# Kernel optimization log

Hardware: AMD Instinct MI355X
Metric: run time of the kernel (lower is better)

The kernel has to match this reference:

```python
import jax, jax.numpy as jnp
import numpy as np

B, C, H, N = 4, 128, 4, 2048
D = C // H  # head_dim = 32
BN_EPS = 1e-5


def _conv1(w, b, x):
    # 1x1 Conv1d: [O,C] x [B,C,N] -> [B,O,N]
    return jnp.einsum('oc,bcn->bon', w, x) + b[None, :, None]


def setup_inputs() -> dict:
    key = jax.random.key(0)
    ks = jax.random.split(key, 20)
    p = lambda k, shape: jax.random.normal(k, shape, dtype=jnp.float32) * 0.05
    return {
        'x1': jax.random.normal(ks[0], (B, C, N), dtype=jnp.float32),
        'x2': jax.random.normal(ks[1], (B, C, N), dtype=jnp.float32),
        'kv_mask': jnp.ones((B, N), dtype=bool),
        'wq': p(ks[2], (C, C)), 'bq': p(ks[3], (C,)),
        'wk': p(ks[4], (C, C)), 'bk': p(ks[5], (C,)),
        'wv': p(ks[6], (C, C)), 'bv': p(ks[7], (C,)),
        'wm': p(ks[8], (C, C)), 'bm': p(ks[9], (C,)),
        'wc1': p(ks[10], (2 * C, 2 * C)), 'bc1': p(ks[11], (2 * C,)),
        'bn_gamma': jnp.ones((2 * C,), dtype=jnp.float32),
        'bn_beta': jnp.zeros((2 * C,), dtype=jnp.float32),
        'bn_mean': p(ks[12], (2 * C,)),
        'bn_var': jax.random.uniform(ks[13], (2 * C,), dtype=jnp.float32, minval=0.5, maxval=1.5),
        'wc2': p(ks[14], (C, 2 * C)), 'bc2': p(ks[15], (C,)),
    }


def reference(x1, x2, kv_mask, wq, bq, wk, bk, wv, bv, wm, bm,
              wc1, bc1, bn_gamma, bn_beta, bn_mean, bn_var, wc2, bc2):
    b, _, n = x1.shape
    q = _conv1(wq, bq, x1).reshape(b, H, D, n)   # bhdn
    k = _conv1(wk, bk, x2).reshape(b, H, D, -1)  # bhdm
    v = _conv1(wv, bv, x2).reshape(b, H, D, -1)  # bhdm
    qk = jnp.einsum('bhdn,bhdm->bhnm', q, k)
    # masked_fill on raw QK before scaling, matching torch code
    qk = jnp.where(kv_mask[:, None, None, :], qk, jnp.float32(-1e6))
    score = jax.nn.softmax(qk * (1.0 / D ** 0.5), axis=-1)
    add_value = jnp.einsum('bhnm,bhdm->bhdn', score, v).reshape(b, C, n)
    add_value = _conv1(wm, bm, add_value)
    cat = jnp.concatenate([x1, add_value], axis=1)  # [B, 2C, N]
    h = _conv1(wc1, bc1, cat)
    # BatchNorm1d in inference mode (running stats)
    h = (h - bn_mean[None, :, None]) * jax.lax.rsqrt(bn_var[None, :, None] + BN_EPS)
    h = h * bn_gamma[None, :, None] + bn_beta[None, :, None]
    h = jax.nn.relu(h)
    h = _conv1(wc2, bc2, h)
    return x1 + h
```

## Files before the change

### kernel.cpp

```cpp
#include <hip/hip_runtime.h>

typedef __attribute__((ext_vector_type(4))) float v4f;
typedef __attribute__((ext_vector_type(8))) _Float16 half8;
typedef __attribute__((ext_vector_type(4))) _Float16 half4;
typedef __attribute__((ext_vector_type(2))) _Float16 half2t;

constexpr float C2 = 0.17677669529663687f * 1.44269504088896341f;

__device__ __forceinline__ half4 pk4(float a, float b, float c, float d) {
  half2t lo = __builtin_bit_cast(half2t, __builtin_amdgcn_cvt_pkrtz(a, b));
  half2t hi = __builtin_bit_cast(half2t, __builtin_amdgcn_cvt_pkrtz(c, d));
  return __builtin_shufflevector(lo, hi, 0, 1, 2, 3);
}
__device__ __forceinline__ half8 pk8f4(const float4 a, const float4 b) {
  const half4 lo = pk4(a.x, a.y, a.z, a.w);
  const half4 hi = pk4(b.x, b.y, b.z, b.w);
  return __builtin_shufflevector(lo, hi, 0, 1, 2, 3, 4, 5, 6, 7);
}

__global__ __launch_bounds__(512) void qkv(
    const float* __restrict__ x1, const float* __restrict__ x2,
    const float* __restrict__ wq, const float* __restrict__ bq,
    const float* __restrict__ wk, const float* __restrict__ bk,
    const float* __restrict__ wv, const float* __restrict__ bv,
    const float* __restrict__ wm, const float* __restrict__ wc1,
    const float* __restrict__ wc2, const unsigned char* __restrict__ mask,
    _Float16* __restrict__ Qpk, _Float16* __restrict__ Kpk,
    _Float16* __restrict__ Vpk, _Float16* __restrict__ wts,
    float* __restrict__ maskf) {
  const int b = blockIdx.y;
  const int bx = blockIdx.x;
  const int tid = threadIdx.x, w = tid >> 6, lane = tid & 63;
  const int l = lane & 15, q = lane >> 4;
  const int n0 = bx * 16;
  const int n = n0 + l;

  __shared__ _Float16 x1s[16 * 136];
  __shared__ _Float16 x2s[16 * 136];

  if (b == 0 && bx < 72) {
    const int e = (bx * 512 + tid) * 4;
    const float* src;
    int base;
    if (e < 16384) { src = wm; base = 0; }
    else if (e < 81920) { src = wc1; base = 16384; }
    else { src = wc2; base = 81920; }
    const float4 t = *(const float4*)(src + (e - base));
    *(half4*)(wts + e) = pk4(t.x, t.y, t.z, t.w);
  } else if (b == 1 && bx < 4) {
    const int e = (bx * 512 + tid) * 4;
    const unsigned mv = *(const unsigned*)(mask + e);
    float4 o;
    o.x = (mv & 0x000000ffu) ? 0.f : -1.0e6f * C2;
    o.y = (mv & 0x0000ff00u) ? 0.f : -1.0e6f * C2;
    o.z = (mv & 0x00ff0000u) ? 0.f : -1.0e6f * C2;
    o.w = (mv & 0xff000000u) ? 0.f : -1.0e6f * C2;
    *(float4*)(maskf + e) = o;
  }

  {
    const int ch = tid >> 2, seg = tid & 3;
    const float4 a = *(const float4*)(x1 + (size_t)(b * 128 + ch) * 2048 + n0 + seg * 4);
    const float4 c = *(const float4*)(x2 + (size_t)(b * 128 + ch) * 2048 + n0 + seg * 4);
    x1s[(seg * 4 + 0) * 136 + ch] = (_Float16)a.x;
    x1s[(seg * 4 + 1) * 136 + ch] = (_Float16)a.y;
    x1s[(seg * 4 + 2) * 136 + ch] = (_Float16)a.z;
    x1s[(seg * 4 + 3) * 136 + ch] = (_Float16)a.w;
    x2s[(seg * 4 + 0) * 136 + ch] = (_Float16)c.x;
    x2s[(seg * 4 + 1) * 136 + ch] = (_Float16)c.y;
    x2s[(seg * 4 + 2) * 136 + ch] = (_Float16)c.z;
    x2s[(seg * 4 + 3) * 136 + ch] = (_Float16)c.w;
  }
  __syncthreads();

  half8 x1f[4], x2f[4];
#pragma unroll
  for (int kt = 0; kt < 4; ++kt) {
    x1f[kt] = *(const half8*)&x1s[l * 136 + kt * 32 + q * 8];
    x2f[kt] = *(const half8*)&x2s[l * 136 + kt * 32 + q * 8];
  }

#pragma unroll
  for (int i = 0; i < 3; ++i) {
    const int t = w * 3 + i;
    if (t < 8) {
      const int mt = t;
      v4f acc = *(const v4f*)(bq + mt * 16 + q * 4);
#pragma unroll
      for (int kt = 0; kt < 4; ++kt) {
        const float4 wa = *(const float4*)(wq + (mt * 16 + l) * 128 + kt * 32 + q * 8);
        const float4 wb = *(const float4*)(wq + (mt * 16 + l) * 128 + kt * 32 + q * 8 + 4);
        acc = __builtin_amdgcn_mfma_f32_16x16x32_f16(pk8f4(wa, wb), x1f[kt], acc, 0, 0, 0);
      }
      *(half4*)(Qpk + ((size_t)(b * 8 + mt) * 2048 + n) * 16 + q * 4) =
          pk4(acc[0] * C2, acc[1] * C2, acc[2] * C2, acc[3] * C2);
    } else if (t < 16) {
      const int mt = t - 8;
      v4f acc = *(const v4f*)(bk + mt * 16 + q * 4);
#pragma unroll
      for (int kt = 0; kt < 4; ++kt) {
        const float4 wa = *(const float4*)(wk + (mt * 16 + l) * 128 + kt * 32 + q * 8);
        const float4 wb = *(const float4*)(wk + (mt * 16 + l) * 128 + kt * 32 + q * 8 + 4);
        acc = __builtin_amdgcn_mfma_f32_16x16x32_f16(pk8f4(wa, wb), x2f[kt], acc, 0, 0, 0);
      }
      *(half4*)(Kpk + ((size_t)(b * 8 + mt) * 2048 + n) * 16 + q * 4) =
          pk4(acc[0], acc[1], acc[2], acc[3]);
    } else {
      const int ot = t - 16;
      const float bvv = bv[ot * 16 + l];
      v4f acc = {bvv, bvv, bvv, bvv};
#pragma unroll
      for (int kt = 0; kt < 4; ++kt) {
        const float4 wa = *(const float4*)(wv + (ot * 16 + l) * 128 + kt * 32 + q * 8);
        const float4 wb = *(const float4*)(wv + (ot * 16 + l) * 128 + kt * 32 + q * 8 + 4);
        acc = __builtin_amdgcn_mfma_f32_16x16x32_f16(x2f[kt], pk8f4(wa, wb), acc, 0, 0, 0);
      }
      *(half4*)(Vpk + (((size_t)(b * 4 + (ot >> 1)) * 128 + bx) * 32 +
                       (ot & 1) * 16 + l) * 16 + q * 4) =
          pk4(acc[0], acc[1], acc[2], acc[3]);
    }
  }
}

__global__ __launch_bounds__(256) void attn(
    const _Float16* __restrict__ Qpk, const _Float16* __restrict__ Kpk,
    const _Float16* __restrict__ Vpk, const float* __restrict__ maskf,
    _Float16* __restrict__ Opk, float* __restrict__ lsump) {
  const int bh = blockIdx.y, b = bh >> 2, h = bh & 3;
  const int part = blockIdx.z;
  const int tid = threadIdx.x, w = tid >> 6, lane = tid & 63;
  const int l = lane & 15, q = lane >> 4;
  const int nb = blockIdx.x * 128 + w * 32;

  __shared__ _Float16 ldsK[2][3088];
  __shared__ _Float16 ldsV[2][3072];

  const size_t qrow = (size_t)(b * 8 + h * 2 + (q >> 1)) * 2048;
  const half8 qf0 = *(const half8*)(Qpk + (qrow + nb + l) * 16 + (q & 1) * 8);
  const half8 qf1 = *(const half8*)(Qpk + (qrow + nb + 16 + l) * 16 + (q & 1) * 8);
  const _Float16* __restrict__ Kg = Kpk + (size_t)(b * 8 + h * 2) * 2048 * 16;
  const _Float16* __restrict__ Vg = Vpk + (size_t)((b * 4 + h) * 128) * 512;
  const float* __restrict__ mf = maskf + b * 2048;

  const int kct = tid >> 7, kk = (tid >> 1) & 63, khf = tid & 1;
  const int vt = tid >> 6, vd = (tid >> 1) & 31;

  v4f oacc[2][2] = {{{0.f, 0.f, 0.f, 0.f}, {0.f, 0.f, 0.f, 0.f}},
                    {{0.f, 0.f, 0.f, 0.f}, {0.f, 0.f, 0.f, 0.f}}};
  float ls0 = 0.f, ls1 = 0.f;
  const int mbeg = part * 512;

  half8 kr = *(const half8*)(Kg + ((size_t)kct * 2048 + mbeg + kk) * 16 + khf * 8);
  half8 vr = *(const half8*)(Vg + (size_t)((mbeg >> 4) + vt) * 512 + vd * 16 + khf * 8);
  *(half8*)&ldsK[0][kct * 1544 + kk * 24 + khf * 8] = kr;
  *(half8*)&ldsV[0][vt * 768 + vd * 24 + khf * 8] = vr;
  __syncthreads();

  for (int i = 0; i < 8; ++i) {
    const int m0 = mbeg + i * 64;
    const int cur = i & 1;
    if (i < 7) {
      kr = *(const half8*)(Kg + ((size_t)kct * 2048 + m0 + 64 + kk) * 16 + khf * 8);
      vr = *(const half8*)(Vg + (size_t)(((m0 + 64) >> 4) + vt) * 512 + vd * 16 + khf * 8);
    }
    half4 pB[2][4];
#pragma unroll
    for (int mt = 0; mt < 4; ++mt) {
      const half8 kf =
          *(const half8*)&ldsK[cur][(q >> 1) * 1544 + (mt * 16 + l) * 24 + (q & 1) * 8];
      const v4f biasv = *(const v4f*)(mf + m0 + mt * 16 + q * 4);
      const v4f s0 = __builtin_amdgcn_mfma_f32_16x16x32_f16(kf, qf0, biasv, 0, 0, 0);
      const v4f s1 = __builtin_amdgcn_mfma_f32_16x16x32_f16(kf, qf1, biasv, 0, 0, 0);
      const float a0 = exp2f(s0[0]), a1 = exp2f(s0[1]), a2 = exp2f(s0[2]),
                  a3 = exp2f(s0[3]);
      const float c0 = exp2f(s1[0]), c1 = exp2f(s1[1]), c2 = exp2f(s1[2]),
                  c3 = exp2f(s1[3]);
      ls0 += (a0 + a1) + (a2 + a3);
      ls1 += (c0 + c1) + (c2 + c3);
      pB[0][mt] = pk4(a0, a1, a2, a3);
      pB[1][mt] = pk4(c0, c1, c2, c3);
    }
#pragma unroll
    for (int mt = 0; mt < 4; ++mt) {
      const half4 vf0 = *(const half4*)&ldsV[cur][mt * 768 + l * 24 + q * 4];
      const half4 vf1 = *(const half4*)&ldsV[cur][mt * 768 + (16 + l) * 24 + q * 4];
      oacc[0][0] = __builtin_amdgcn_mfma_f32_16x16x16f16(vf0, pB[0][mt], oacc[0][0], 0, 0, 0);
      oacc[0][1] = __builtin_amdgcn_mfma_f32_16x16x16f16(vf1, pB[0][mt], oacc[0][1], 0, 0, 0);
      oacc[1][0] = __builtin_amdgcn_mfma_f32_16x16x16f16(vf0, pB[1][mt], oacc[1][0], 0, 0, 0);
      oacc[1][1] = __builtin_amdgcn_mfma_f32_16x16x16f16(vf1, pB[1][mt], oacc[1][1], 0, 0, 0);
    }
    if (i < 7) {
      *(half8*)&ldsK[cur ^ 1][kct * 1544 + kk * 24 + khf * 8] = kr;
      *(half8*)&ldsV[cur ^ 1][vt * 768 + vd * 24 + khf * 8] = vr;
      __syncthreads();
    }
  }
  ls0 += __shfl_xor(ls0, 16);
  ls0 += __shfl_xor(ls0, 32);
  ls1 += __shfl_xor(ls1, 16);
  ls1 += __shfl_xor(ls1, 32);
  if (q == 0) {
    lsump[part * 32768 + bh * 2048 + nb + l] = ls0;
    lsump[part * 32768 + bh * 2048 + nb + 16 + l] = ls1;
  }
#pragma unroll
  for (int qt = 0; qt < 2; ++qt)
#pragma unroll
    for (int df = 0; df < 2; ++df)
      *(half4*)(Opk + (size_t)part * 1048576 +
                ((size_t)(b * 8 + h * 2 + df) * 2048 + nb + qt * 16 + l) * 16 +
                q * 4) = pk4(oacc[qt][df][0], oacc[qt][df][1], oacc[qt][df][2],
                             oacc[qt][df][3]);
}

__global__ __launch_bounds__(512) void post(
    const float* __restrict__ x1, const _Float16* __restrict__ Opk,
    const float* __restrict__ lsump, const _Float16* __restrict__ wts,
    const float* __restrict__ bm, const float* __restrict__ bc1,
    const float* __restrict__ gamma, const float* __restrict__ beta,
    const float* __restrict__ mean, const float* __restrict__ var,
    const float* __restrict__ bc2, float* __restrict__ out) {
  const int b = blockIdx.y;
  const int n0 = blockIdx.x * 16;
  const int tid = threadIdx.x, w = tid >> 6, lane = tid & 63;
  const int l = lane & 15, q = lane >> 4;
  const int n = n0 + l;
  const _Float16* wm_h = wts;
  const _Float16* wc1_h = wts + 16384;
  const _Float16* wc2_h = wts + 81920;

  __shared__ _Float16 exA[8 * 256];
  __shared__ _Float16 exB[16 * 256];

  float rlh[4];
#pragma unroll
  for (int hh = 0; hh < 4; ++hh) {
    const size_t idx = (size_t)(b * 4 + hh) * 2048 + n;
    rlh[hh] = 1.0f / (lsump[idx] + lsump[32768 + idx] + lsump[65536 + idx] +
                      lsump[98304 + idx]);
  }
  half4 of[8];
#pragma unroll
  for (int kt = 0; kt < 8; ++kt) {
    const size_t oa = ((size_t)(b * 8 + kt) * 2048 + n) * 16 + q * 4;
    const half4 a = *(const half4*)(Opk + oa);
    const half4 c = *(const half4*)(Opk + 1048576 + oa);
    const half4 d = *(const half4*)(Opk + 2097152 + oa);
    const half4 e = *(const half4*)(Opk + 3145728 + oa);
    const _Float16 rh = (_Float16)rlh[kt >> 1];
    const half4 rl4 = {rh, rh, rh, rh};
    of[kt] = ((a + c) + (d + e)) * rl4;
  }
  half4 catf[16];
  float xr[4];
#pragma unroll
  for (int kt = 0; kt < 8; ++kt) {
    const float v0 = x1[(size_t)(b * 128 + kt * 16 + q * 4 + 0) * 2048 + n];
    const float v1 = x1[(size_t)(b * 128 + kt * 16 + q * 4 + 1) * 2048 + n];
    const float v2 = x1[(size_t)(b * 128 + kt * 16 + q * 4 + 2) * 2048 + n];
    const float v3 = x1[(size_t)(b * 128 + kt * 16 + q * 4 + 3) * 2048 + n];
    if (kt == w) { xr[0] = v0; xr[1] = v1; xr[2] = v2; xr[3] = v3; }
    catf[kt] = pk4(v0, v1, v2, v3);
  }
  {
    v4f acc = *(const v4f*)(bm + w * 16 + q * 4);
#pragma unroll
    for (int kt = 0; kt < 8; ++kt) {
      const half4 wf = *(const half4*)(wm_h + (w * 16 + l) * 128 + kt * 16 + q * 4);
      acc = __builtin_amdgcn_mfma_f32_16x16x16f16(wf, of[kt], acc, 0, 0, 0);
    }
    *(half4*)&exA[w * 256 + l * 16 + q * 4] = pk4(acc[0], acc[1], acc[2], acc[3]);
  }
  __syncthreads();
#pragma unroll
  for (int f = 0; f < 8; ++f)
    catf[8 + f] = *(const half4*)&exA[f * 256 + l * 16 + q * 4];
#pragma unroll
  for (int i = 0; i < 2; ++i) {
    const int mt = w * 2 + i;
    v4f acc = *(const v4f*)(bc1 + mt * 16 + q * 4);
#pragma unroll
    for (int kt = 0; kt < 16; ++kt) {
      const half4 wf = *(const half4*)(wc1_h + (mt * 16 + l) * 256 + kt * 16 + q * 4);
      acc = __builtin_amdgcn_mfma_f32_16x16x16f16(wf, catf[kt], acc, 0, 0, 0);
    }
    const v4f g = *(const v4f*)(gamma + mt * 16 + q * 4);
    const v4f bt = *(const v4f*)(beta + mt * 16 + q * 4);
    const v4f mn = *(const v4f*)(mean + mt * 16 + q * 4);
    const v4f vr = *(const v4f*)(var + mt * 16 + q * 4);
    float hh[4];
#pragma unroll
    for (int r = 0; r < 4; ++r) {
      const float a1 = g[r] * rsqrtf(vr[r] + 1e-5f);
      const float b1 = bt[r] - mn[r] * a1;
      hh[r] = fmaxf(acc[r] * a1 + b1, 0.f);
    }
    *(half4*)&exB[mt * 256 + l * 16 + q * 4] = pk4(hh[0], hh[1], hh[2], hh[3]);
  }
  __syncthreads();
  {
    v4f acc = *(const v4f*)(bc2 + w * 16 + q * 4);
#pragma unroll
    for (int kt = 0; kt < 16; ++kt) {
      const half4 hfv = *(const half4*)&exB[kt * 256 + l * 16 + q * 4];
      const half4 wf = *(const half4*)(wc2_h + (w * 16 + l) * 256 + kt * 16 + q * 4);
      acc = __builtin_amdgcn_mfma_f32_16x16x16f16(wf, hfv, acc, 0, 0, 0);
    }
#pragma unroll
    for (int r = 0; r < 4; ++r)
      out[(size_t)(b * 128 + w * 16 + q * 4 + r) * 2048 + n] = acc[r] + xr[r];
  }
}

extern "C" void kernel_launch(void* const* d_in, const int* in_sizes, int n_in,
                              void* d_out, int out_size, void* d_ws,
                              size_t ws_size, hipStream_t stream) {
  const float* x1 = (const float*)d_in[0];
  const float* x2 = (const float*)d_in[1];
  const unsigned char* kv_mask = (const unsigned char*)d_in[2];
  const float* wq = (const float*)d_in[3];
  const float* bq = (const float*)d_in[4];
  const float* wk = (const float*)d_in[5];
  const float* bk = (const float*)d_in[6];
  const float* wv = (const float*)d_in[7];
  const float* bv = (const float*)d_in[8];
  const float* wm = (const float*)d_in[9];
  const float* bm = (const float*)d_in[10];
  const float* wc1 = (const float*)d_in[11];
  const float* bc1 = (const float*)d_in[12];
  const float* bn_gamma = (const float*)d_in[13];
  const float* bn_beta = (const float*)d_in[14];
  const float* bn_mean = (const float*)d_in[15];
  const float* bn_var = (const float*)d_in[16];
  const float* wc2 = (const float*)d_in[17];
  const float* bc2 = (const float*)d_in[18];
  float* out = (float*)d_out;

  char* p = (char*)d_ws;
  _Float16* Qpk = (_Float16*)p;
  _Float16* Kpk = (_Float16*)(p + (size_t)2 * 1024 * 1024);
  _Float16* Vpk = (_Float16*)(p + (size_t)4 * 1024 * 1024);
  _Float16* Opk = (_Float16*)(p + (size_t)6 * 1024 * 1024);
  _Float16* wts = (_Float16*)(p + (size_t)14 * 1024 * 1024);
  float* lsump = (float*)(p + (size_t)14 * 1024 * 1024 + 512 * 1024);
  float* maskf = lsump + 4 * 32768;

  qkv<<<dim3(128, 4), 512, 0, stream>>>(x1, x2, wq, bq, wk, bk, wv, bv, wm,
                                        wc1, wc2, kv_mask, Qpk, Kpk, Vpk, wts,
                                        maskf);
  attn<<<dim3(16, 16, 4), 256, 0, stream>>>(Qpk, Kpk, Vpk, maskf, Opk, lsump);
  post<<<dim3(128, 4), 512, 0, stream>>>(x1, Opk, lsump, wts, bm, bc1,
                                         bn_gamma, bn_beta, bn_mean, bn_var,
                                         bc2, out);
}
```

Before: 167.6 us.

## Stage x1 and combined attention output through LDS in post; prioritize MFMA

In the post kernel, each block now loads its x1 tile once with float4 reads, transposes it into shared memory, and has each wave combine one slice of the four attention partials into shared memory. Previously every wave redundantly loaded all of x1 and all partials with scalar strided reads. This removes duplicated global traffic at the cost of extra LDS space and a barrier. Separately, the attention loop wraps its MFMA sections in s_setprio hints so matrix issue is favored over the exp and LDS work of other waves.

```diff
diff --git a/kernel.cpp b/kernel.cpp
--- a/kernel.cpp
+++ b/kernel.cpp
@@ -169,8 +169,10 @@
       const half8 kf =
           *(const half8*)&ldsK[cur][(q >> 1) * 1544 + (mt * 16 + l) * 24 + (q & 1) * 8];
       const v4f biasv = *(const v4f*)(mf + m0 + mt * 16 + q * 4);
+      __builtin_amdgcn_s_setprio(1);
       const v4f s0 = __builtin_amdgcn_mfma_f32_16x16x32_f16(kf, qf0, biasv, 0, 0, 0);
       const v4f s1 = __builtin_amdgcn_mfma_f32_16x16x32_f16(kf, qf1, biasv, 0, 0, 0);
+      __builtin_amdgcn_s_setprio(0);
       const float a0 = exp2f(s0[0]), a1 = exp2f(s0[1]), a2 = exp2f(s0[2]),
                   a3 = exp2f(s0[3]);
       const float c0 = exp2f(s1[0]), c1 = exp2f(s1[1]), c2 = exp2f(s1[2]),
@@ -180,6 +182,7 @@
       pB[0][mt] = pk4(a0, a1, a2, a3);
       pB[1][mt] = pk4(c0, c1, c2, c3);
     }
+    __builtin_amdgcn_s_setprio(1);
 #pragma unroll
     for (int mt = 0; mt < 4; ++mt) {
       const half4 vf0 = *(const half4*)&ldsV[cur][mt * 768 + l * 24 + q * 4];
@@ -189,6 +192,7 @@
       oacc[1][0] = __builtin_amdgcn_mfma_f32_16x16x16f16(vf0, pB[1][mt], oacc[1][0], 0, 0, 0);
       oacc[1][1] = __builtin_amdgcn_mfma_f32_16x16x16f16(vf1, pB[1][mt], oacc[1][1], 0, 0, 0);
     }
+    __builtin_amdgcn_s_setprio(0);
     if (i < 7) {
       *(half8*)&ldsK[cur ^ 1][kct * 1544 + kk * 24 + khf * 8] = kr;
       *(half8*)&ldsV[cur ^ 1][vt * 768 + vd * 24 + khf * 8] = vr;
@@ -229,38 +233,45 @@
   const _Float16* wc1_h = wts + 16384;
   const _Float16* wc2_h = wts + 81920;
 
-  __shared__ _Float16 exA[8 * 256];
-  __shared__ _Float16 exB[16 * 256];
-
-  float rlh[4];
-#pragma unroll
-  for (int hh = 0; hh < 4; ++hh) {
-    const size_t idx = (size_t)(b * 4 + hh) * 2048 + n;
-    rlh[hh] = 1.0f / (lsump[idx] + lsump[32768 + idx] + lsump[65536 + idx] +
-                      lsump[98304 + idx]);
-  }
-  half4 of[8];
-#pragma unroll
-  for (int kt = 0; kt < 8; ++kt) {
-    const size_t oa = ((size_t)(b * 8 + kt) * 2048 + n) * 16 + q * 4;
+  __shared__ __align__(16) float x1s[16 * 132];
+  __shared__ __align__(16) _Float16 ofs[8 * 256];
+  __shared__ __align__(16) _Float16 exA[8 * 256];
+  __shared__ __align__(16) _Float16 exB[16 * 256];
+
+  {
+    const int ch = tid >> 2, seg = tid & 3;
+    const float4 a = *(const float4*)(x1 + (size_t)(b * 128 + ch) * 2048 + n0 + seg * 4);
+    x1s[(seg * 4 + 0) * 132 + ch] = a.x;
+    x1s[(seg * 4 + 1) * 132 + ch] = a.y;
+    x1s[(seg * 4 + 2) * 132 + ch] = a.z;
+    x1s[(seg * 4 + 3) * 132 + ch] = a.w;
+  }
+  {
+    const size_t idx = (size_t)(b * 4 + (w >> 1)) * 2048 + n;
+    const float rl = 1.0f / (lsump[idx] + lsump[32768 + idx] +
+                             lsump[65536 + idx] + lsump[98304 + idx]);
+    const size_t oa = ((size_t)(b * 8 + w) * 2048 + n) * 16 + q * 4;
     const half4 a = *(const half4*)(Opk + oa);
     const half4 c = *(const half4*)(Opk + 1048576 + oa);
     const half4 d = *(const half4*)(Opk + 2097152 + oa);
     const half4 e = *(const half4*)(Opk + 3145728 + oa);
-    const _Float16 rh = (_Float16)rlh[kt >> 1];
+    const _Float16 rh = (_Float16)rl;
     const half4 rl4 = {rh, rh, rh, rh};
-    of[kt] = ((a + c) + (d + e)) * rl4;
-  }
+    *(half4*)&ofs[w * 256 + l * 16 + q * 4] = ((a + c) + (d + e)) * rl4;
+  }
+  __syncthreads();
+
+  half4 of[8];
+#pragma unroll
+  for (int kt = 0; kt < 8; ++kt)
+    of[kt] = *(const half4*)&ofs[kt * 256 + l * 16 + q * 4];
   half4 catf[16];
   float xr[4];
 #pragma unroll
   for (int kt = 0; kt < 8; ++kt) {
-    const float v0 = x1[(size_t)(b * 128 + kt * 16 + q * 4 + 0) * 2048 + n];
-    const float v1 = x1[(size_t)(b * 128 + kt * 16 + q * 4 + 1) * 2048 + n];
-    const float v2 = x1[(size_t)(b * 128 + kt * 16 + q * 4 + 2) * 2048 + n];
-    const float v3 = x1[(size_t)(b * 128 + kt * 16 + q * 4 + 3) * 2048 + n];
-    if (kt == w) { xr[0] = v0; xr[1] = v1; xr[2] = v2; xr[3] = v3; }
-    catf[kt] = pk4(v0, v1, v2, v3);
+    const float4 xv = *(const float4*)&x1s[l * 132 + kt * 16 + q * 4];
+    if (kt == w) { xr[0] = xv.x; xr[1] = xv.y; xr[2] = xv.z; xr[3] = xv.w; }
+    catf[kt] = pk4(xv.x, xv.y, xv.z, xv.w);
   }
   {
     v4f acc = *(const v4f*)(bm + w * 16 + q * 4);
```

New measurement: 162.5 us. 1.03x faster.
